# Optimization experiments

Measured on AMD Instinct MI355X. Metric: run time of the kernel, lower is better.

Reference implementation:

```python
import jax, jax.numpy as jnp
import numpy as np

B, N, T, ET = 256, 256, 100, 4
MSG_HID, MSG_OUT, N_HID, N_CLASSES = 128, 64, 64, 2
N_EDGES = N * (N - 1) // 2  # 32640


def _xavier(k, out_dim, in_dim):
    std = (2.0 / (in_dim + out_dim)) ** 0.5
    return jax.random.normal(k, (out_dim, in_dim), dtype=jnp.float32) * std


def setup_inputs() -> dict:
    key = jax.random.key(0)
    ks = jax.random.split(key, 7)
    return {
        "inputs": jax.random.normal(ks[0], (B, N, T), dtype=jnp.float32),
        "sparse_edges": jax.random.uniform(ks[1], (B, N_EDGES, ET), dtype=jnp.float32),
        "w1": _xavier(ks[2], MSG_HID, N), "b1": jnp.full((MSG_HID,), 0.1, jnp.float32),
        "w2": _xavier(ks[3], MSG_OUT, MSG_HID), "b2": jnp.full((MSG_OUT,), 0.1, jnp.float32),
        "wo1": _xavier(ks[4], N_HID, MSG_OUT), "bo1": jnp.full((N_HID,), 0.1, jnp.float32),
        "wo2": _xavier(ks[5], N_HID, N_HID), "bo2": jnp.full((N_HID,), 0.1, jnp.float32),
        "wo3": _xavier(ks[6], N_CLASSES, N_HID), "bo3": jnp.full((N_CLASSES,), 0.1, jnp.float32),
    }


def reference(inputs, sparse_edges, w1, b1, w2, b2, wo1, bo1, wo2, bo2, wo3, bo3):
    b, n, _ = inputs.shape
    r, c = np.triu_indices(n, k=1)  # static index pattern
    # Scatter all non-null edge types at once: [B, ET-1, N, N]
    se = jnp.swapaxes(sparse_edges[:, :, 1:], 1, 2)  # [B, ET-1, E]
    adj = jnp.zeros((b, se.shape[1], n, n), dtype=se.dtype)
    adj = adj.at[:, :, r, c].set(se)
    adj = adj + jnp.swapaxes(adj, -1, -2)  # symmetrize
    # Message MLP (dropout_prob = 0 -> identity)
    h = jax.nn.relu(jnp.einsum('beij,hj->beih', adj, w1) + b1)   # [B,ET-1,N,msg_hid]
    m = jax.nn.relu(jnp.einsum('beih,oh->beio', h, w2) + b2)     # [B,ET-1,N,msg_out]
    # Weighted sum over edge types: weight for type i is i*0.2, i=1..ET-1
    wts = (jnp.arange(1, sparse_edges.shape[2]) * 0.2).astype(m.dtype)
    out = jnp.einsum('beio,e->bio', m, wts)                      # [B,N,msg_out]
    # Output head
    p = jax.nn.relu(out @ wo1.T + bo1)
    p = jax.nn.relu(p @ wo2.T + bo2)
    p = jnp.mean(p, axis=1)  # mean over atoms
    return p @ wo3.T + bo3   # [B, n_classes]
```

## Files before the change

kernel.cpp:

```cpp
#include <hip/hip_runtime.h>

#define N_ 256
#define E_ 32640

typedef __bf16 bf16x8 __attribute__((ext_vector_type(8)));
typedef float f32x4 __attribute__((ext_vector_type(4)));

__device__ __forceinline__ unsigned short cvt1(float f) {
  return __builtin_bit_cast(unsigned short, (__bf16)f);
}

__device__ __forceinline__ bf16x8 ldfrag(const unsigned short* base, int row, int kbyte, int rowbytes) {
  int byte = (row * rowbytes + kbyte) ^ ((row & 7) << 4);
  return *reinterpret_cast<const bf16x8*>(reinterpret_cast<const char*>(base) + byte);
}

__device__ __forceinline__ void st2(unsigned short* base, int row, int colbyte, int rowbytes, unsigned short v) {
  int byte = (row * rowbytes + colbyte) ^ ((row & 7) << 4);
  *reinterpret_cast<unsigned short*>(reinterpret_cast<char*>(base) + byte) = v;
}

__device__ __forceinline__ void stA3(unsigned short* sA0, int lr, int cb, float4 v) {
  int byte = (lr * 512 + cb) ^ ((lr & 7) << 4);
  char* p = reinterpret_cast<char*>(sA0) + byte;
  *reinterpret_cast<unsigned short*>(p)         = cvt1(v.y);
  *reinterpret_cast<unsigned short*>(p + 16384) = cvt1(v.z);
  *reinterpret_cast<unsigned short*>(p + 32768) = cvt1(v.w);
}

__device__ __forceinline__ bf16x8 pack8(float4 lo, float4 hi) {
  bf16x8 r;
  r[0] = (__bf16)lo.x; r[1] = (__bf16)lo.y; r[2] = (__bf16)lo.z; r[3] = (__bf16)lo.w;
  r[4] = (__bf16)hi.x; r[5] = (__bf16)hi.y; r[6] = (__bf16)hi.z; r[7] = (__bf16)hi.w;
  return r;
}

__global__ __launch_bounds__(512, 4) void chunk_kernel(
    const float* __restrict__ se_g,
    const float* __restrict__ w1,  const float* __restrict__ b1,
    const float* __restrict__ w2,  const float* __restrict__ b2,
    const float* __restrict__ wo1, const float* __restrict__ bo1,
    const float* __restrict__ wo2, const float* __restrict__ bo2,
    float* __restrict__ ws)
{
  __shared__ __align__(16) unsigned short sA[3 * 32 * N_];
  __shared__ __align__(16) unsigned short sH3[3 * 32 * 128];
  __shared__ float sAccW[8][64];

  const int tid = threadIdx.x;
  const int i   = blockIdx.x;
  const int batch = (i & 7) * 32 + ((i >> 3) & 31);
  const int chunk = i >> 8;
  const int r0    = chunk * 32;

  const int w   = tid >> 6;
  const int l   = tid & 63;
  const int l15 = l & 15;
  const int lk  = l >> 4;
  const int kb0 = lk * 16;

  const int c1 = w;
  const int r2 = w >> 2;
  const int c2 = w & 3;

  reinterpret_cast<float*>(sAccW)[tid] = 0.f;

  bf16x8 W1f[8];
  {
    const float* p = w1 + (c1 * 16 + l15) * 256 + lk * 8;
    #pragma unroll
    for (int ks = 0; ks < 8; ++ks) {
      float4 lo = *reinterpret_cast<const float4*>(p + ks * 32);
      float4 hi = *reinterpret_cast<const float4*>(p + ks * 32 + 4);
      W1f[ks] = pack8(lo, hi);
    }
  }
  bf16x8 W2f[4];
  {
    const float* p = w2 + (c2 * 16 + l15) * 128 + lk * 8;
    #pragma unroll
    for (int ks = 0; ks < 4; ++ks) {
      float4 lo = *reinterpret_cast<const float4*>(p + ks * 32);
      float4 hi = *reinterpret_cast<const float4*>(p + ks * 32 + 4);
      W2f[ks] = pack8(lo, hi);
    }
  }

  const float4* seB = reinterpret_cast<const float4*>(se_g) + (size_t)batch * E_;

  {
    const int span0 = (r0 * (511 - r0)) >> 1;
    const int S     = (((r0 + 32) * (479 - r0)) >> 1) - span0;
    int t = tid;
    float4 p0 = {}, p1 = {};
    if (t < S)       p0 = seB[span0 + t];
    if (t + 512 < S) p1 = seB[span0 + t + 512];
    for (; t < S; t += 512) {
      float4 v = p0;
      p0 = p1;
      if (t + 1024 < S) p1 = seB[span0 + t + 1024];
      int g = span0 + t;
      float disc = (float)(261121 - 8 * g);
      int gi = (int)((511.0f - sqrtf(disc)) * 0.5f);
      while (gi * (511 - gi) > 2 * g) --gi;
      while ((gi + 1) * (510 - gi) <= 2 * g) ++gi;
      int j = g - ((gi * (511 - gi)) >> 1) + gi + 1;
      stA3(sA, gi - r0, j * 2, v);
    }
  }
  {
    const int sub = tid >> 5, l32 = tid & 31;
    const int K = (r0 + 31 + 15) >> 4;
    for (int k0 = 0; k0 < K; k0 += 4) {
      float4 v[4]; int lr[4], cb[4]; bool ok[4];
      #pragma unroll
      for (int kk = 0; kk < 4; ++kk) {
        int j   = sub + ((k0 + kk) << 4);
        int i0  = (j + 1 > r0) ? (j + 1) : r0;
        int cnt = r0 + 32 - i0;
        int ii  = i0 + l32;
        bool val = (j < r0 + 31) && (l32 < cnt);
        int u = j * 255 - ((j * (j - 1)) >> 1) + (ii - j - 1);
        ok[kk] = val; lr[kk] = ii - r0; cb[kk] = j * 2;
        v[kk] = seB[val ? u : 0];
      }
      #pragma unroll
      for (int kk = 0; kk < 4; ++kk)
        if (ok[kk]) stA3(sA, lr[kk], cb[kk], v[kk]);
    }
  }
  if (tid < 32) {
    int byte = (tid * 512 + (r0 + tid) * 2) ^ ((tid & 7) << 4);
    char* p = reinterpret_cast<char*>(sA) + byte;
    *reinterpret_cast<unsigned short*>(p)         = 0;
    *reinterpret_cast<unsigned short*>(p + 16384) = 0;
    *reinterpret_cast<unsigned short*>(p + 32768) = 0;
  }
  __syncthreads();

  {
    const float bias = b1[c1 * 16 + l15];
    #pragma unroll
    for (int e = 0; e < 3; ++e) {
      f32x4 acc0 = {0,0,0,0}, acc1 = {0,0,0,0};
      const unsigned short* sAe = sA + e * (32 * N_);
      #pragma unroll
      for (int ks = 0; ks < 8; ++ks) {
        int kb = ks * 64 + kb0;
        bf16x8 a0 = ldfrag(sAe, l15,      kb, 512);
        bf16x8 a1 = ldfrag(sAe, 16 + l15, kb, 512);
        acc0 = __builtin_amdgcn_mfma_f32_16x16x32_bf16(a0, W1f[ks], acc0, 0, 0, 0);
        acc1 = __builtin_amdgcn_mfma_f32_16x16x32_bf16(a1, W1f[ks], acc1, 0, 0, 0);
      }
      unsigned short* sHe = sH3 + e * (32 * 128);
      int cc = c1 * 16 + l15;
      #pragma unroll
      for (int r = 0; r < 4; ++r) {
        st2(sHe, lk * 4 + r,      cc * 2, 256, cvt1(fmaxf(acc0[r] + bias, 0.f)));
        st2(sHe, 16 + lk * 4 + r, cc * 2, 256, cvt1(fmaxf(acc1[r] + bias, 0.f)));
      }
    }
  }
  __syncthreads();

  unsigned short* sX = sA;
  unsigned short* sP = sA + 2048;
  bf16x8 WO1f[2], WO2f[2];
  {
    f32x4 outAcc = {0,0,0,0};
    const float bias = b2[c2 * 16 + l15];
    int arow = r2 * 16 + l15;
    #pragma unroll
    for (int e = 0; e < 3; ++e) {
      f32x4 acc = {0,0,0,0};
      const unsigned short* sHe = sH3 + e * (32 * 128);
      #pragma unroll
      for (int ks = 0; ks < 4; ++ks) {
        bf16x8 a = ldfrag(sHe, arow, ks * 64 + kb0, 256);
        acc = __builtin_amdgcn_mfma_f32_16x16x32_bf16(a, W2f[ks], acc, 0, 0, 0);
      }
      float wte = 0.2f * (float)(e + 1);
      #pragma unroll
      for (int r = 0; r < 4; ++r)
        outAcc[r] += wte * fmaxf(acc[r] + bias, 0.f);
    }
    {
      const float* p1 = wo1 + (c2 * 16 + l15) * 64 + lk * 8;
      const float* p2 = wo2 + (c2 * 16 + l15) * 64 + lk * 8;
      #pragma unroll
      for (int ks = 0; ks < 2; ++ks) {
        WO1f[ks] = pack8(*reinterpret_cast<const float4*>(p1 + ks * 32),
                         *reinterpret_cast<const float4*>(p1 + ks * 32 + 4));
        WO2f[ks] = pack8(*reinterpret_cast<const float4*>(p2 + ks * 32),
                         *reinterpret_cast<const float4*>(p2 + ks * 32 + 4));
      }
    }
    int col = c2 * 16 + l15;
    #pragma unroll
    for (int r = 0; r < 4; ++r)
      st2(sX, r2 * 16 + lk * 4 + r, col * 2, 128, cvt1(outAcc[r]));
  }
  __syncthreads();

  {
    const float bias = bo1[c2 * 16 + l15];
    f32x4 acc = {0,0,0,0};
    int arow = r2 * 16 + l15;
    #pragma unroll
    for (int ks = 0; ks < 2; ++ks) {
      bf16x8 a = ldfrag(sX, arow, ks * 64 + kb0, 128);
      acc = __builtin_amdgcn_mfma_f32_16x16x32_bf16(a, WO1f[ks], acc, 0, 0, 0);
    }
    #pragma unroll
    for (int r = 0; r < 4; ++r)
      st2(sP, r2 * 16 + lk * 4 + r, (c2 * 16 + l15) * 2, 128, cvt1(fmaxf(acc[r] + bias, 0.f)));
  }
  __syncthreads();

  {
    const float bias = bo2[c2 * 16 + l15];
    f32x4 acc = {0,0,0,0};
    int arow = r2 * 16 + l15;
    #pragma unroll
    for (int ks = 0; ks < 2; ++ks) {
      bf16x8 a = ldfrag(sP, arow, ks * 64 + kb0, 128);
      acc = __builtin_amdgcn_mfma_f32_16x16x32_bf16(a, WO2f[ks], acc, 0, 0, 0);
    }
    float s = 0.f;
    #pragma unroll
    for (int r = 0; r < 4; ++r) s += fmaxf(acc[r] + bias, 0.f);
    s += __shfl_xor(s, 16);
    s += __shfl_xor(s, 32);
    if (lk == 0) sAccW[w][c2 * 16 + l15] = s;
  }
  __syncthreads();

  if (tid < 64) {
    float s = 0.f;
    #pragma unroll
    for (int ww = 0; ww < 8; ++ww) s += sAccW[ww][tid];
    ws[((size_t)batch * 8 + chunk) * 64 + tid] = s;
  }
}

__global__ __launch_bounds__(512) void finish_kernel(
    const float* __restrict__ ws,
    const float* __restrict__ wo3, const float* __restrict__ bo3,
    float* __restrict__ out)
{
  int b = blockIdx.x * 8 + (threadIdx.x >> 6);
  int l = threadIdx.x & 63;
  float s = 0.f;
  #pragma unroll
  for (int c = 0; c < 8; ++c) s += ws[((size_t)b * 8 + c) * 64 + l];
  s *= (1.0f / 256.0f);
  float v0 = s * wo3[l];
  float v1 = s * wo3[64 + l];
  #pragma unroll
  for (int off = 32; off > 0; off >>= 1) {
    v0 += __shfl_down(v0, off);
    v1 += __shfl_down(v1, off);
  }
  if (l == 0) {
    out[b * 2 + 0] = v0 + bo3[0];
    out[b * 2 + 1] = v1 + bo3[1];
  }
}

extern "C" void kernel_launch(void* const* d_in, const int* in_sizes, int n_in,
                              void* d_out, int out_size, void* d_ws, size_t ws_size,
                              hipStream_t stream) {
  (void)in_sizes; (void)n_in; (void)ws_size; (void)out_size;
  const float* se  = (const float*)d_in[1];
  const float* w1  = (const float*)d_in[2];
  const float* b1  = (const float*)d_in[3];
  const float* w2  = (const float*)d_in[4];
  const float* b2  = (const float*)d_in[5];
  const float* wo1 = (const float*)d_in[6];
  const float* bo1 = (const float*)d_in[7];
  const float* wo2 = (const float*)d_in[8];
  const float* bo2 = (const float*)d_in[9];
  const float* wo3 = (const float*)d_in[10];
  const float* bo3 = (const float*)d_in[11];
  float* ws = (float*)d_ws;
  chunk_kernel<<<dim3(2048), dim3(512), 0, stream>>>(
      se, w1, b1, w2, b2, wo1, bo1, wo2, bo2, ws);
  finish_kernel<<<dim3(32), dim3(512), 0, stream>>>(ws, wo3, bo3, (float*)d_out);
}
```

Measured before the change: 108.0 us.

## Make chunk kernel persistent over 16-row chunks with prefetch and warp specialization

Each block now handles half a batch (eight 16-row chunks) in a loop instead of one 32-row chunk per block. It prefetches the next chunk's upper-triangle edges into registers while computing the current layer-1 MFMAs. During the head stage, the non-head warps stage the lower-triangle data for the next chunk. Grid size drops from 2048 to 512 blocks, shared memory per block roughly halves, and launch bounds change to 2 blocks per CU. The aim is to hide global-load latency behind compute and cut the idle head warps, at the cost of fewer, longer-running blocks, more register pressure from the prefetch buffer, and more barriers per block.

Result: faster. 103.8 us (-3.9%).

```diff
diff --git a/kernel.cpp b/kernel.cpp
--- a/kernel.cpp
+++ b/kernel.cpp
@@ -1,6 +1,5 @@
 #include <hip/hip_runtime.h>
 
-#define N_ 256
 #define E_ 32640
 
 typedef __bf16 bf16x8 __attribute__((ext_vector_type(8)));
@@ -14,20 +13,17 @@
   int byte = (row * rowbytes + kbyte) ^ ((row & 7) << 4);
   return *reinterpret_cast<const bf16x8*>(reinterpret_cast<const char*>(base) + byte);
 }
-
 __device__ __forceinline__ void st2(unsigned short* base, int row, int colbyte, int rowbytes, unsigned short v) {
   int byte = (row * rowbytes + colbyte) ^ ((row & 7) << 4);
   *reinterpret_cast<unsigned short*>(reinterpret_cast<char*>(base) + byte) = v;
 }
-
 __device__ __forceinline__ void stA3(unsigned short* sA0, int lr, int cb, float4 v) {
   int byte = (lr * 512 + cb) ^ ((lr & 7) << 4);
   char* p = reinterpret_cast<char*>(sA0) + byte;
   *reinterpret_cast<unsigned short*>(p)         = cvt1(v.y);
-  *reinterpret_cast<unsigned short*>(p + 16384) = cvt1(v.z);
-  *reinterpret_cast<unsigned short*>(p + 32768) = cvt1(v.w);
-}
-
+  *reinterpret_cast<unsigned short*>(p + 8192)  = cvt1(v.z);
+  *reinterpret_cast<unsigned short*>(p + 16384) = cvt1(v.w);
+}
 __device__ __forceinline__ bf16x8 pack8(float4 lo, float4 hi) {
   bf16x8 r;
   r[0] = (__bf16)lo.x; r[1] = (__bf16)lo.y; r[2] = (__bf16)lo.z; r[3] = (__bf16)lo.w;
@@ -35,7 +31,57 @@
   return r;
 }
 
-__global__ __launch_bounds__(512, 4) void chunk_kernel(
+__device__ __forceinline__ int ubase(int i) { return (i * (511 - i)) >> 1; }
+
+__device__ __forceinline__ void decode_g(int g, int& gi, int& j) {
+  float disc = (float)(261121 - 8 * g);
+  int t = (int)((511.0f - sqrtf(disc)) * 0.5f);
+  while (t * (511 - t) > 2 * g) --t;
+  while ((t + 1) * (510 - t) <= 2 * g) ++t;
+  gi = t;
+  j = g - ((t * (511 - t)) >> 1) + t + 1;
+}
+
+__device__ __forceinline__ void stage_lower(const float4* seB, unsigned short* sA,
+                                            int r0, int glane, int ngroups) {
+  const int sub = glane >> 4, l16 = glane & 15;
+  const int nStrips = r0 + 15;
+  for (int j0 = sub; j0 < nStrips; j0 += ngroups * 4) {
+    float4 v[4]; int lr[4], cb[4]; bool ok[4];
+    #pragma unroll
+    for (int kk = 0; kk < 4; ++kk) {
+      int j  = j0 + kk * ngroups;
+      int i0 = (j + 1 > r0) ? (j + 1) : r0;
+      int cnt = r0 + 16 - i0;
+      int ii = i0 + l16;
+      bool val = (j < nStrips) && (l16 < cnt);
+      int u = j * 255 - ((j * (j - 1)) >> 1) + (ii - j - 1);
+      ok[kk] = val; lr[kk] = ii - r0; cb[kk] = j * 2;
+      v[kk] = seB[val ? u : 0];
+    }
+    #pragma unroll
+    for (int kk = 0; kk < 4; ++kk)
+      if (ok[kk]) stA3(sA, lr[kk], cb[kk], v[kk]);
+  }
+}
+
+__device__ __forceinline__ void stage_upper_sync(const float4* seB, unsigned short* sA,
+                                                 int r0, int tid) {
+  const int s0 = ubase(r0);
+  const int S  = ubase(r0 + 16) - s0;
+  int t = tid;
+  float4 p0 = {}, p1 = {};
+  if (t < S)       p0 = seB[s0 + t];
+  if (t + 512 < S) p1 = seB[s0 + t + 512];
+  for (; t < S; t += 512) {
+    float4 v = p0; p0 = p1;
+    if (t + 1024 < S) p1 = seB[s0 + t + 1024];
+    int gi, j; decode_g(s0 + t, gi, j);
+    stA3(sA, gi - r0, j * 2, v);
+  }
+}
+
+__global__ __launch_bounds__(512, 2) void chunk_kernel(
     const float* __restrict__ se_g,
     const float* __restrict__ w1,  const float* __restrict__ b1,
     const float* __restrict__ w2,  const float* __restrict__ b2,
@@ -43,15 +89,17 @@
     const float* __restrict__ wo2, const float* __restrict__ bo2,
     float* __restrict__ ws)
 {
-  __shared__ __align__(16) unsigned short sA[3 * 32 * N_];
-  __shared__ __align__(16) unsigned short sH3[3 * 32 * 128];
-  __shared__ float sAccW[8][64];
+  __shared__ __align__(16) unsigned short sA[3 * 16 * 256];
+  __shared__ __align__(16) unsigned short sH3[3 * 16 * 128];
+  __shared__ __align__(16) unsigned short sXP[2 * 16 * 64];
+  __shared__ float sAccC[64];
 
   const int tid = threadIdx.x;
   const int i   = blockIdx.x;
-  const int batch = (i & 7) * 32 + ((i >> 3) & 31);
-  const int chunk = i >> 8;
-  const int r0    = chunk * 32;
+  const int half  = i >> 8;
+  const int within = i & 255;
+  const int batch = (within & 7) * 32 + (within >> 3);
+  const int cbase = half * 8;
 
   const int w   = tid >> 6;
   const int l   = tid & 63;
@@ -60,187 +108,167 @@
   const int kb0 = lk * 16;
 
   const int c1 = w;
-  const int r2 = w >> 2;
   const int c2 = w & 3;
-
-  reinterpret_cast<float*>(sAccW)[tid] = 0.f;
+  const bool isHead = (w < 4);
+
+  if (tid < 64) sAccC[tid] = 0.f;
 
   bf16x8 W1f[8];
   {
     const float* p = w1 + (c1 * 16 + l15) * 256 + lk * 8;
     #pragma unroll
-    for (int ks = 0; ks < 8; ++ks) {
-      float4 lo = *reinterpret_cast<const float4*>(p + ks * 32);
-      float4 hi = *reinterpret_cast<const float4*>(p + ks * 32 + 4);
-      W1f[ks] = pack8(lo, hi);
-    }
+    for (int ks = 0; ks < 8; ++ks)
+      W1f[ks] = pack8(*reinterpret_cast<const float4*>(p + ks * 32),
+                      *reinterpret_cast<const float4*>(p + ks * 32 + 4));
   }
   bf16x8 W2f[4];
   {
     const float* p = w2 + (c2 * 16 + l15) * 128 + lk * 8;
     #pragma unroll
-    for (int ks = 0; ks < 4; ++ks) {
-      float4 lo = *reinterpret_cast<const float4*>(p + ks * 32);
-      float4 hi = *reinterpret_cast<const float4*>(p + ks * 32 + 4);
-      W2f[ks] = pack8(lo, hi);
-    }
-  }
+    for (int ks = 0; ks < 4; ++ks)
+      W2f[ks] = pack8(*reinterpret_cast<const float4*>(p + ks * 32),
+                      *reinterpret_cast<const float4*>(p + ks * 32 + 4));
+  }
+  const float b1v  = b1[c1 * 16 + l15];
+  const float b2v  = b2[c2 * 16 + l15];
+  const float bo1v = bo1[c2 * 16 + l15];
+  const float bo2v = bo2[c2 * 16 + l15];
 
   const float4* seB = reinterpret_cast<const float4*>(se_g) + (size_t)batch * E_;
+  unsigned short* sX = sXP;
+  unsigned short* sP = sXP + 16 * 64;
 
   {
-    const int span0 = (r0 * (511 - r0)) >> 1;
-    const int S     = (((r0 + 32) * (479 - r0)) >> 1) - span0;
-    int t = tid;
-    float4 p0 = {}, p1 = {};
-    if (t < S)       p0 = seB[span0 + t];
-    if (t + 512 < S) p1 = seB[span0 + t + 512];
-    for (; t < S; t += 512) {
-      float4 v = p0;
-      p0 = p1;
-      if (t + 1024 < S) p1 = seB[span0 + t + 1024];
-      int g = span0 + t;
-      float disc = (float)(261121 - 8 * g);
-      int gi = (int)((511.0f - sqrtf(disc)) * 0.5f);
-      while (gi * (511 - gi) > 2 * g) --gi;
-      while ((gi + 1) * (510 - gi) <= 2 * g) ++gi;
-      int j = g - ((gi * (511 - gi)) >> 1) + gi + 1;
-      stA3(sA, gi - r0, j * 2, v);
-    }
-  }
-  {
-    const int sub = tid >> 5, l32 = tid & 31;
-    const int K = (r0 + 31 + 15) >> 4;
-    for (int k0 = 0; k0 < K; k0 += 4) {
-      float4 v[4]; int lr[4], cb[4]; bool ok[4];
-      #pragma unroll
-      for (int kk = 0; kk < 4; ++kk) {
-        int j   = sub + ((k0 + kk) << 4);
-        int i0  = (j + 1 > r0) ? (j + 1) : r0;
-        int cnt = r0 + 32 - i0;
-        int ii  = i0 + l32;
-        bool val = (j < r0 + 31) && (l32 < cnt);
-        int u = j * 255 - ((j * (j - 1)) >> 1) + (ii - j - 1);
-        ok[kk] = val; lr[kk] = ii - r0; cb[kk] = j * 2;
-        v[kk] = seB[val ? u : 0];
-      }
-      #pragma unroll
-      for (int kk = 0; kk < 4; ++kk)
-        if (ok[kk]) stA3(sA, lr[kk], cb[kk], v[kk]);
-    }
-  }
-  if (tid < 32) {
-    int byte = (tid * 512 + (r0 + tid) * 2) ^ ((tid & 7) << 4);
-    char* p = reinterpret_cast<char*>(sA) + byte;
-    *reinterpret_cast<unsigned short*>(p)         = 0;
-    *reinterpret_cast<unsigned short*>(p + 16384) = 0;
-    *reinterpret_cast<unsigned short*>(p + 32768) = 0;
+    int r0 = cbase * 16;
+    stage_upper_sync(seB, sA, r0, tid);
+    stage_lower(seB, sA, r0, tid, 32);
+    if (tid < 16) {
+      int byte = (tid * 512 + (r0 + tid) * 2) ^ ((tid & 7) << 4);
+      char* p = reinterpret_cast<char*>(sA) + byte;
+      *reinterpret_cast<unsigned short*>(p)         = 0;
+      *reinterpret_cast<unsigned short*>(p + 8192)  = 0;
+      *reinterpret_cast<unsigned short*>(p + 16384) = 0;
+    }
   }
   __syncthreads();
 
-  {
-    const float bias = b1[c1 * 16 + l15];
-    #pragma unroll
-    for (int e = 0; e < 3; ++e) {
-      f32x4 acc0 = {0,0,0,0}, acc1 = {0,0,0,0};
-      const unsigned short* sAe = sA + e * (32 * N_);
-      #pragma unroll
-      for (int ks = 0; ks < 8; ++ks) {
-        int kb = ks * 64 + kb0;
-        bf16x8 a0 = ldfrag(sAe, l15,      kb, 512);
-        bf16x8 a1 = ldfrag(sAe, 16 + l15, kb, 512);
-        acc0 = __builtin_amdgcn_mfma_f32_16x16x32_bf16(a0, W1f[ks], acc0, 0, 0, 0);
-        acc1 = __builtin_amdgcn_mfma_f32_16x16x32_bf16(a1, W1f[ks], acc1, 0, 0, 0);
-      }
-      unsigned short* sHe = sH3 + e * (32 * 128);
-      int cc = c1 * 16 + l15;
-      #pragma unroll
-      for (int r = 0; r < 4; ++r) {
-        st2(sHe, lk * 4 + r,      cc * 2, 256, cvt1(fmaxf(acc0[r] + bias, 0.f)));
-        st2(sHe, 16 + lk * 4 + r, cc * 2, 256, cvt1(fmaxf(acc1[r] + bias, 0.f)));
-      }
-    }
-  }
-  __syncthreads();
-
-  unsigned short* sX = sA;
-  unsigned short* sP = sA + 2048;
-  bf16x8 WO1f[2], WO2f[2];
-  {
-    f32x4 outAcc = {0,0,0,0};
-    const float bias = b2[c2 * 16 + l15];
-    int arow = r2 * 16 + l15;
-    #pragma unroll
-    for (int e = 0; e < 3; ++e) {
-      f32x4 acc = {0,0,0,0};
-      const unsigned short* sHe = sH3 + e * (32 * 128);
-      #pragma unroll
-      for (int ks = 0; ks < 4; ++ks) {
-        bf16x8 a = ldfrag(sHe, arow, ks * 64 + kb0, 256);
-        acc = __builtin_amdgcn_mfma_f32_16x16x32_bf16(a, W2f[ks], acc, 0, 0, 0);
-      }
-      float wte = 0.2f * (float)(e + 1);
+  for (int cc = 0; cc < 8; ++cc) {
+    const int r0 = (cbase + cc) * 16;
+    const bool more = (cc < 7);
+    const int nr0 = r0 + 16;
+
+    float4 pf[8];
+    int s0 = 0, S = 0;
+    if (more) {
+      s0 = ubase(nr0);
+      S  = ubase(nr0 + 16) - s0;
+      #pragma unroll
+      for (int k = 0; k < 8; ++k) {
+        int t = tid + k * 512;
+        pf[k] = seB[s0 + (t < S ? t : 0)];
+      }
+    }
+
+    {
+      const int ccol = c1 * 16 + l15;
+      #pragma unroll
+      for (int e = 0; e < 3; ++e) {
+        f32x4 acc = {0, 0, 0, 0};
+        const unsigned short* sAe = sA + e * 4096;
+        #pragma unroll
+        for (int ks = 0; ks < 8; ++ks)
+          acc = __builtin_amdgcn_mfma_f32_16x16x32_bf16(
+              ldfrag(sAe, l15, ks * 64 + kb0, 512), W1f[ks], acc, 0, 0, 0);
+        unsigned short* sHe = sH3 + e * 2048;
+        #pragma unroll
+        for (int r = 0; r < 4; ++r)
+          st2(sHe, lk * 4 + r, ccol * 2, 256, cvt1(fmaxf(acc[r] + b1v, 0.f)));
+      }
+    }
+    __syncthreads();
+
+    if (more) {
+      #pragma unroll
+      for (int k = 0; k < 8; ++k) {
+        int t = tid + k * 512;
+        if (t < S) {
+          int gi, j; decode_g(s0 + t, gi, j);
+          stA3(sA, gi - nr0, j * 2, pf[k]);
+        }
+      }
+      if (tid < 16) {
+        int byte = (tid * 512 + (nr0 + tid) * 2) ^ ((tid & 7) << 4);
+        char* p = reinterpret_cast<char*>(sA) + byte;
+        *reinterpret_cast<unsigned short*>(p)         = 0;
+        *reinterpret_cast<unsigned short*>(p + 8192)  = 0;
+        *reinterpret_cast<unsigned short*>(p + 16384) = 0;
+      }
+    }
+    bf16x8 WO1f[2], WO2f[2];
+    if (isHead) {
+      const float* q1 = wo1 + (c2 * 16 + l15) * 64 + lk * 8;
+      const float* q2 = wo2 + (c2 * 16 + l15) * 64 + lk * 8;
+      float4 wa0 = *reinterpret_cast<const float4*>(q1);
+      float4 wa1 = *reinterpret_cast<const float4*>(q1 + 4);
+      float4 wa2 = *reinterpret_cast<const float4*>(q1 + 32);
+      float4 wa3 = *reinterpret_cast<const float4*>(q1 + 36);
+      float4 wb0 = *reinterpret_cast<const float4*>(q2);
+      float4 wb1 = *reinterpret_cast<const float4*>(q2 + 4);
+      float4 wb2 = *reinterpret_cast<const float4*>(q2 + 32);
+      float4 wb3 = *reinterpret_cast<const float4*>(q2 + 36);
+      f32x4 outAcc = {0, 0, 0, 0};
+      #pragma unroll
+      for (int e = 0; e < 3; ++e) {
+        f32x4 acc = {0, 0, 0, 0};
+        const unsigned short* sHe = sH3 + e * 2048;
+        #pragma unroll
+        for (int ks = 0; ks < 4; ++ks)
+          acc = __builtin_amdgcn_mfma_f32_16x16x32_bf16(
+              ldfrag(sHe, l15, ks * 64 + kb0, 256), W2f[ks], acc, 0, 0, 0);
+        float wte = 0.2f * (float)(e + 1);
+        #pragma unroll
+        for (int r = 0; r < 4; ++r)
+          outAcc[r] += wte * fmaxf(acc[r] + b2v, 0.f);
+      }
+      WO1f[0] = pack8(wa0, wa1); WO1f[1] = pack8(wa2, wa3);
+      WO2f[0] = pack8(wb0, wb1); WO2f[1] = pack8(wb2, wb3);
       #pragma unroll
       for (int r = 0; r < 4; ++r)
-        outAcc[r] += wte * fmaxf(acc[r] + bias, 0.f);
-    }
-    {
-      const float* p1 = wo1 + (c2 * 16 + l15) * 64 + lk * 8;
-      const float* p2 = wo2 + (c2 * 16 + l15) * 64 + lk * 8;
-      #pragma unroll
-      for (int ks = 0; ks < 2; ++ks) {
-        WO1f[ks] = pack8(*reinterpret_cast<const float4*>(p1 + ks * 32),
-                         *reinterpret_cast<const float4*>(p1 + ks * 32 + 4));
-        WO2f[ks] = pack8(*reinterpret_cast<const float4*>(p2 + ks * 32),
-                         *reinterpret_cast<const float4*>(p2 + ks * 32 + 4));
-      }
-    }
-    int col = c2 * 16 + l15;
-    #pragma unroll
-    for (int r = 0; r < 4; ++r)
-      st2(sX, r2 * 16 + lk * 4 + r, col * 2, 128, cvt1(outAcc[r]));
-  }
-  __syncthreads();
-
-  {
-    const float bias = bo1[c2 * 16 + l15];
-    f32x4 acc = {0,0,0,0};
-    int arow = r2 * 16 + l15;
-    #pragma unroll
-    for (int ks = 0; ks < 2; ++ks) {
-      bf16x8 a = ldfrag(sX, arow, ks * 64 + kb0, 128);
-      acc = __builtin_amdgcn_mfma_f32_16x16x32_bf16(a, WO1f[ks], acc, 0, 0, 0);
-    }
-    #pragma unroll
-    for (int r = 0; r < 4; ++r)
-      st2(sP, r2 * 16 + lk * 4 + r, (c2 * 16 + l15) * 2, 128, cvt1(fmaxf(acc[r] + bias, 0.f)));
-  }
-  __syncthreads();
-
-  {
-    const float bias = bo2[c2 * 16 + l15];
-    f32x4 acc = {0,0,0,0};
-    int arow = r2 * 16 + l15;
-    #pragma unroll
-    for (int ks = 0; ks < 2; ++ks) {
-      bf16x8 a = ldfrag(sP, arow, ks * 64 + kb0, 128);
-      acc = __builtin_amdgcn_mfma_f32_16x16x32_bf16(a, WO2f[ks], acc, 0, 0, 0);
-    }
-    float s = 0.f;
-    #pragma unroll
-    for (int r = 0; r < 4; ++r) s += fmaxf(acc[r] + bias, 0.f);
-    s += __shfl_xor(s, 16);
-    s += __shfl_xor(s, 32);
-    if (lk == 0) sAccW[w][c2 * 16 + l15] = s;
-  }
-  __syncthreads();
-
-  if (tid < 64) {
-    float s = 0.f;
-    #pragma unroll
-    for (int ww = 0; ww < 8; ++ww) s += sAccW[ww][tid];
-    ws[((size_t)batch * 8 + chunk) * 64 + tid] = s;
-  }
+        st2(sX, lk * 4 + r, (c2 * 16 + l15) * 2, 128, cvt1(outAcc[r]));
+    } else if (more) {
+      stage_lower(seB, sA, nr0, tid - 256, 16);
+    }
+    __syncthreads();
+
+    if (isHead) {
+      f32x4 acc = {0, 0, 0, 0};
+      #pragma unroll
+      for (int ks = 0; ks < 2; ++ks)
+        acc = __builtin_amdgcn_mfma_f32_16x16x32_bf16(
+            ldfrag(sX, l15, ks * 64 + kb0, 128), WO1f[ks], acc, 0, 0, 0);
+      #pragma unroll
+      for (int r = 0; r < 4; ++r)
+        st2(sP, lk * 4 + r, (c2 * 16 + l15) * 2, 128, cvt1(fmaxf(acc[r] + bo1v, 0.f)));
+    }
+    __syncthreads();
+
+    if (isHead) {
+      f32x4 acc = {0, 0, 0, 0};
+      #pragma unroll
+      for (int ks = 0; ks < 2; ++ks)
+        acc = __builtin_amdgcn_mfma_f32_16x16x32_bf16(
+            ldfrag(sP, l15, ks * 64 + kb0, 128), WO2f[ks], acc, 0, 0, 0);
+      float s = 0.f;
+      #pragma unroll
+      for (int r = 0; r < 4; ++r) s += fmaxf(acc[r] + bo2v, 0.f);
+      s += __shfl_xor(s, 16);
+      s += __shfl_xor(s, 32);
+      if (lk == 0) sAccC[c2 * 16 + l15] += s;
+    }
+    __syncthreads();
+  }
+
+  if (tid < 64) ws[((size_t)batch * 2 + half) * 64 + tid] = sAccC[tid];
 }
 
 __global__ __launch_bounds__(512) void finish_kernel(
@@ -250,10 +278,7 @@
 {
   int b = blockIdx.x * 8 + (threadIdx.x >> 6);
   int l = threadIdx.x & 63;
-  float s = 0.f;
-  #pragma unroll
-  for (int c = 0; c < 8; ++c) s += ws[((size_t)b * 8 + c) * 64 + l];
-  s *= (1.0f / 256.0f);
+  float s = (ws[((size_t)b * 2 + 0) * 64 + l] + ws[((size_t)b * 2 + 1) * 64 + l]) * (1.0f / 256.0f);
   float v0 = s * wo3[l];
   float v1 = s * wo3[64 + l];
   #pragma unroll
@@ -283,7 +308,7 @@
   const float* wo3 = (const float*)d_in[10];
   const float* bo3 = (const float*)d_in[11];
   float* ws = (float*)d_ws;
-  chunk_kernel<<<dim3(2048), dim3(512), 0, stream>>>(
+  chunk_kernel<<<dim3(512), dim3(512), 0, stream>>>(
       se, w1, b1, w2, b2, wo1, bo1, wo2, bo2, ws);
   finish_kernel<<<dim3(32), dim3(512), 0, stream>>>(ws, wo3, bo3, (float*)d_out);
 }
```
